# Kernel tuning notes

Measured on AMD Instinct MI355X. Metric: run time of the kernel, lower is better.

Reference implementation:

```python
import jax, jax.numpy as jnp
import numpy as np

N_NODES = 10000
N_EDGES = 320000
N_GRAPHS = 64
L = 3  # num_layers


def _gru(a, h, wih, whh, bih, bhh):
    # torch.nn.GRUCell math: input a, hidden h
    gi = a @ wih.T + bih
    gh = h @ whh.T + bhh
    ir, iz, inn = jnp.split(gi, 3, axis=-1)
    hr, hz, hn = jnp.split(gh, 3, axis=-1)
    r = jax.nn.sigmoid(ir + hr)
    z = jax.nn.sigmoid(iz + hz)
    n = jnp.tanh(inn + r * hn)
    return (1.0 - z) * n + z * h


def _ggc(x, src, dst, w, wih, whh, bih, bhh):
    # PyG GatedGraphConv: pad features up to out_channels, then L rounds of
    # (linear -> scatter-add over edges -> GRUCell update)
    out_ch = w.shape[-1]
    if x.shape[-1] < out_ch:
        x = jnp.concatenate(
            [x, jnp.zeros((x.shape[0], out_ch - x.shape[-1]), x.dtype)], axis=-1)
    for i in range(w.shape[0]):
        m = x @ w[i]                                        # [N, C]
        a = jax.ops.segment_sum(m[src], dst, num_segments=N_NODES)  # scatter-add
        x = _gru(a, x, wih, whh, bih, bhh)
    return x


def setup_inputs() -> dict:
    key = jax.random.key(0)
    ks = jax.random.split(key, 16)
    d1, d2 = 128, 256
    s1, s2 = 1.0 / np.sqrt(d1), 1.0 / np.sqrt(d2)
    x = jax.random.normal(ks[0], (N_NODES, d1), dtype=jnp.float32)
    edge_index = jax.random.randint(ks[1], (2, N_EDGES), 0, N_NODES, dtype=jnp.int64)
    batch = jnp.sort(jax.random.randint(ks[2], (N_NODES,), 0, N_GRAPHS, dtype=jnp.int64))
    return {
        "x": x,
        "edge_index": edge_index,
        "batch": batch,
        "w1": jax.random.normal(ks[3], (L, d1, d1), jnp.float32) * s1,
        "gru1_wih": jax.random.normal(ks[4], (3 * d1, d1), jnp.float32) * s1,
        "gru1_whh": jax.random.normal(ks[5], (3 * d1, d1), jnp.float32) * s1,
        "gru1_bih": jax.random.normal(ks[6], (3 * d1,), jnp.float32) * s1,
        "gru1_bhh": jax.random.normal(ks[7], (3 * d1,), jnp.float32) * s1,
        "w2": jax.random.normal(ks[8], (L, d2, d2), jnp.float32) * s2,
        "gru2_wih": jax.random.normal(ks[9], (3 * d2, d2), jnp.float32) * s2,
        "gru2_whh": jax.random.normal(ks[10], (3 * d2, d2), jnp.float32) * s2,
        "gru2_bih": jax.random.normal(ks[11], (3 * d2,), jnp.float32) * s2,
        "gru2_bhh": jax.random.normal(ks[12], (3 * d2,), jnp.float32) * s2,
        "fc_w": jax.random.normal(ks[13], (6, d2), jnp.float32) * s2,
        "fc_b": jnp.zeros((6,), jnp.float32),
    }


def reference(x, edge_index, batch, w1, gru1_wih, gru1_whh, gru1_bih, gru1_bhh,
              w2, gru2_wih, gru2_whh, gru2_bih, gru2_bhh, fc_w, fc_b):
    src, dst = edge_index[0], edge_index[1]
    y = jax.nn.relu(_ggc(x, src, dst, w1, gru1_wih, gru1_whh, gru1_bih, gru1_bhh))
    y = _ggc(y, src, dst, w2, gru2_wih, gru2_whh, gru2_bih, gru2_bhh)
    y = jax.ops.segment_max(y, batch, num_segments=N_GRAPHS)  # global max pool [G, 256]
    return y @ fc_w.T + fc_b  # [G, 6]
```

## Files before the change

kernel.cpp:

```cpp
#include <hip/hip_runtime.h>

#define NN 10000
#define NNP 10112
#define NE 320000
#define NG 64
#define D1 128
#define D2 256
#define MT 79
#define MT64 158

typedef unsigned short u16;
typedef short v8s __attribute__((ext_vector_type(8)));
typedef float v4f __attribute__((ext_vector_type(4)));

__device__ __forceinline__ u16 f2bf(float x) {
    unsigned u = __float_as_uint(x);
    return (u16)((u + 0x7fffu + ((u >> 16) & 1u)) >> 16);
}
__device__ __forceinline__ float bf2f(u16 b) {
    return __uint_as_float(((unsigned)b) << 16);
}
__device__ __forceinline__ float sigm(float x) { return 1.f / (1.f + __expf(-x)); }
__device__ __forceinline__ float tanh_f(float x) {
    float cx = fminf(fmaxf(x, -15.f), 15.f);
    float e = __expf(2.f * cx);
    return (e - 1.f) / (e + 1.f);
}

#define MF(d, a, b) d = __builtin_amdgcn_mfma_f32_16x16x32_bf16(a, b, d, 0, 0, 0)

#define GLDS16(gp, lp)                                                         \
    __builtin_amdgcn_global_load_lds(                                          \
        (__attribute__((address_space(1))) unsigned int*)(unsigned long long)(gp), \
        (__attribute__((address_space(3))) unsigned int*)(lp), 16, 0, 0)

#define SWIZZLE(bx, by)                          \
    const int bid_ = blockIdx.x;                 \
    const int l_ = bid_ >> 3;                    \
    const int by = (bid_ & 7) * 10 + l_ % 10;    \
    const int bx = l_ / 10;                      \
    if (by >= MT) return;

__global__ __launch_bounds__(256)
void mm_k(const u16* __restrict__ Ah, const u16* __restrict__ Al,
          const u16* __restrict__ Bh, const u16* __restrict__ Bl,
          float* __restrict__ Cm, int K) {
    const int by = blockIdx.x, bx = blockIdx.y;
    __shared__ u16 lds[16384];
    const int tid = threadIdx.x;
    const int wave = tid >> 6, lane = tid & 63;
    const int wm = (wave >> 1) * 32, wn = (wave & 1) * 32;
    const int bm = by * 64, bn = bx * 64;
    const int quad = lane >> 4, r16 = lane & 15;
    const int NK = K >> 5;

    auto STAGE = [&](int b, int k0) {
        size_t ga = (size_t)(bm + lane) * K + k0 + wave * 8;
        size_t gb = (size_t)(bn + lane) * K + k0 + wave * 8;
        int s = b * 8192 + (wave * 64 + lane) * 8;
        GLDS16(Ah + ga, &lds[s]);
        GLDS16(Al + ga, &lds[2048 + s]);
        GLDS16(Bh + gb, &lds[4096 + s]);
        GLDS16(Bl + gb, &lds[6144 + s]);
    };

    v4f acc[2][2] = {};
    STAGE(0, 0);
    __syncthreads();
    int cur = 0;
    for (int ks = 0; ks < NK; ++ks) {
        if (ks + 1 < NK) STAGE(cur ^ 1, (ks + 1) * 32);
        const int bb = cur * 8192;
        v8s af[2], alf[2], bf[2], blf[2];
#pragma unroll
        for (int i = 0; i < 2; ++i) {
            int ra = bb + (quad * 64 + wm + i * 16 + r16) * 8;
            int rb = bb + (quad * 64 + wn + i * 16 + r16) * 8;
            af[i]  = *(const v8s*)&lds[ra];
            alf[i] = *(const v8s*)&lds[2048 + ra];
            bf[i]  = *(const v8s*)&lds[4096 + rb];
            blf[i] = *(const v8s*)&lds[6144 + rb];
        }
#pragma unroll
        for (int i = 0; i < 2; ++i)
#pragma unroll
            for (int j = 0; j < 2; ++j) {
                MF(acc[i][j], af[i], bf[j]);
                MF(acc[i][j], af[i], blf[j]);
                MF(acc[i][j], alf[i], bf[j]);
            }
        __syncthreads();
        cur ^= 1;
    }
#pragma unroll
    for (int i = 0; i < 2; ++i) {
        int gr0 = bm + wm + i * 16 + quad * 4;
#pragma unroll
        for (int j = 0; j < 2; ++j) {
            int gc = bn + wn + j * 16 + r16;
#pragma unroll
            for (int r = 0; r < 4; ++r) {
                int gr = gr0 + r;
                if (gr < NN) Cm[(size_t)gr * K + gc] = acc[i][j][r];
            }
        }
    }
}

template<int MODE, int OS>
__global__ __launch_bounds__(256)
void giqru_k(const u16* __restrict__ Ah, const u16* __restrict__ Al,
             const u16* __restrict__ Xh, const u16* __restrict__ Xl,
             const u16* __restrict__ WcH, const u16* __restrict__ WcL,
             const float* __restrict__ bih, const float* __restrict__ bhh,
             u16* __restrict__ xh_out, u16* __restrict__ xl_out,
             const int* __restrict__ batch, unsigned* __restrict__ pool,
             int C) {
    SWIZZLE(bx, by)
    __shared__ u16 lds[32768];
    const int tid = threadIdx.x;
    const int wave = tid >> 6, lane = tid & 63;
    const int wm = (wave >> 1) * 64, wn = (wave & 1) * 64;
    const int bm = by * 128, bn = bx * 128;
    const int quad = lane >> 4, r16 = lane & 15;
    const int K2 = 2 * C;
    const int NK = K2 >> 5;

    auto STAGE = [&](int b, int k0) {
        const u16* sh = (k0 < C) ? Ah : Xh;
        const u16* sl = (k0 < C) ? Al : Xl;
        const int kk = (k0 < C) ? k0 : k0 - C;
        const int bb = b * 16384;
#pragma unroll
        for (int j = 0; j < 2; ++j) {
            int row = j * 64 + lane;
            size_t ga = (size_t)(bm + row) * C + kk + wave * 8;
            size_t gb = (size_t)(bn + row) * K2 + k0 + wave * 8;
            int s = bb + (wave * 128 + row) * 8;
            GLDS16(sh + ga, &lds[s]);
            GLDS16(sl + ga, &lds[4096 + s]);
            GLDS16(WcH + gb, &lds[8192 + s]);
            GLDS16(WcL + gb, &lds[12288 + s]);
        }
    };

    v4f acc[4][4] = {};
    STAGE(0, 0);
    __syncthreads();
    int cur = 0;
    for (int ks = 0; ks < NK; ++ks) {
        if (ks + 1 < NK) STAGE(cur ^ 1, (ks + 1) * 32);
        const int bb = cur * 16384;
        v8s bhf[4], blf[4];
#pragma unroll
        for (int j = 0; j < 4; ++j) {
            int rb = bb + (quad * 128 + wn + j * 16 + r16) * 8;
            bhf[j] = *(const v8s*)&lds[8192 + rb];
            blf[j] = *(const v8s*)&lds[12288 + rb];
        }
        const bool aphase = (ks * 32) < C;
#pragma unroll
        for (int i = 0; i < 4; ++i) {
            int ra = bb + (quad * 128 + wm + i * 16 + r16) * 8;
            v8s fah = *(const v8s*)&lds[ra];
            v8s fal = *(const v8s*)&lds[4096 + ra];
            MF(acc[i][0], fah, bhf[0]); MF(acc[i][0], fah, blf[0]); MF(acc[i][0], fal, bhf[0]);
            MF(acc[i][1], fah, bhf[1]); MF(acc[i][1], fah, blf[1]); MF(acc[i][1], fal, bhf[1]);
            if (aphase) {
                MF(acc[i][2], fah, bhf[2]); MF(acc[i][2], fah, blf[2]); MF(acc[i][2], fal, bhf[2]);
            } else {
                MF(acc[i][3], fah, bhf[3]); MF(acc[i][3], fah, blf[3]); MF(acc[i][3], fal, bhf[3]);
            }
        }
        __syncthreads();
        cur ^= 1;
    }

    const int c = bx * 32 + (wn ? 16 : 0) + r16;
    const float br = bih[c] + bhh[c];
    const float bz = bih[C + c] + bhh[C + c];
    const float bi_n = bih[2 * C + c];
    const float bh_n = bhh[2 * C + c];
#pragma unroll
    for (int i = 0; i < 4; ++i) {
        int R0 = bm + wm + i * 16 + quad * 4;
#pragma unroll
        for (int r = 0; r < 4; ++r) {
            int R = R0 + r;
            if (R >= NN) continue;
            float rr = sigm(acc[i][0][r] + br);
            float zz = sigm(acc[i][1][r] + bz);
            float nn_ = tanh_f(acc[i][2][r] + bi_n + rr * (acc[i][3][r] + bh_n));
            float h = bf2f(Xh[(size_t)R * C + c]) + bf2f(Xl[(size_t)R * C + c]);
            float o = (1.f - zz) * nn_ + zz * h;
            if (MODE == 2) {
                unsigned b = __float_as_uint(o);
                unsigned u = (b & 0x80000000u) ? ~b : (b | 0x80000000u);
                atomicMax(&pool[batch[R] * 256 + c], u);
            } else {
                if (MODE == 1) o = fmaxf(o, 0.f);
                u16 hh = f2bf(o);
                xh_out[(size_t)R * OS + c] = hh;
                xl_out[(size_t)R * OS + c] = f2bf(o - bf2f(hh));
            }
        }
    }
}

__global__ void count_k(const int* __restrict__ dst, int* __restrict__ cnt) {
    int e = blockIdx.x * blockDim.x + threadIdx.x;
    if (e < NE) atomicAdd(&cnt[dst[e]], 1);
}

__global__ void scan_k(const int* __restrict__ cnt, int* __restrict__ off,
                       int* __restrict__ cur) {
    __shared__ int ps[1024];
    const int tid = threadIdx.x;
    const int CH = (NN + 1023) / 1024;
    const int base = tid * CH;
    int s = 0;
    for (int i = 0; i < CH; ++i) {
        int idx = base + i;
        if (idx < NN) s += cnt[idx];
    }
    ps[tid] = s;
    __syncthreads();
    for (int d = 1; d < 1024; d <<= 1) {
        int v = (tid >= d) ? ps[tid - d] : 0;
        __syncthreads();
        ps[tid] += v;
        __syncthreads();
    }
    int run = (tid > 0) ? ps[tid - 1] : 0;
    for (int i = 0; i < CH; ++i) {
        int idx = base + i;
        if (idx <= NN) { off[idx] = run; if (idx < NN) cur[idx] = run; }
        if (idx < NN) run += cnt[idx];
    }
}

__global__ void fill_k(const int* __restrict__ src, const int* __restrict__ dst,
                       int* __restrict__ cur, int* __restrict__ elist) {
    int e = blockIdx.x * blockDim.x + threadIdx.x;
    if (e >= NE) return;
    int p = atomicAdd(&cur[dst[e]], 1);
    elist[p] = src[e];
}

template<int C>
__global__ void gather_k(const float* __restrict__ m, const int* __restrict__ off,
                         const int* __restrict__ elist,
                         u16* __restrict__ ah, u16* __restrict__ al) {
    constexpr int LPN = C / 4;
    int t = blockIdx.x * blockDim.x + threadIdx.x;
    int node = t / LPN;
    if (node >= NN) return;
    int c = (t % LPN) * 4;
    int s0 = off[node], s1 = off[node + 1];
    v4f a0 = 0.f, a1 = 0.f, a2 = 0.f, a3 = 0.f;
    int i = s0;
    for (; i + 4 <= s1; i += 4) {
        int e0 = elist[i], e1 = elist[i + 1], e2 = elist[i + 2], e3 = elist[i + 3];
        v4f v0 = *(const v4f*)(m + (size_t)e0 * C + c);
        v4f v1 = *(const v4f*)(m + (size_t)e1 * C + c);
        v4f v2 = *(const v4f*)(m + (size_t)e2 * C + c);
        v4f v3 = *(const v4f*)(m + (size_t)e3 * C + c);
        a0 += v0; a1 += v1; a2 += v2; a3 += v3;
    }
    for (; i < s1; ++i) {
        int e = elist[i];
        a0 += *(const v4f*)(m + (size_t)e * C + c);
    }
    v4f acc = (a0 + a1) + (a2 + a3);
    ushort4 h, l;
    h.x = f2bf(acc[0]); l.x = f2bf(acc[0] - bf2f(h.x));
    h.y = f2bf(acc[1]); l.y = f2bf(acc[1] - bf2f(h.y));
    h.z = f2bf(acc[2]); l.z = f2bf(acc[2] - bf2f(h.z));
    h.w = f2bf(acc[3]); l.w = f2bf(acc[3] - bf2f(h.w));
    *(ushort4*)(ah + (size_t)node * C + c) = h;
    *(ushort4*)(al + (size_t)node * C + c) = l;
}

__global__ void prep_k(const float* __restrict__ w1, const float* __restrict__ w2,
                       const float* __restrict__ wih1, const float* __restrict__ whh1,
                       const float* __restrict__ wih2, const float* __restrict__ whh2,
                       const float* __restrict__ xin,
                       u16* __restrict__ B1h, u16* __restrict__ B1l,
                       u16* __restrict__ B2h, u16* __restrict__ B2l,
                       u16* __restrict__ Wc1h, u16* __restrict__ Wc1l,
                       u16* __restrict__ Wc2h, u16* __restrict__ Wc2l,
                       u16* __restrict__ xh, u16* __restrict__ xl) {
    const int n1 = 3 * D1 * D1;
    const int n2 = 3 * D2 * D2;
    const int c1 = 4 * D1 * 2 * D1;
    const int c2 = 4 * D2 * 2 * D2;
    int t = blockIdx.x * blockDim.x + threadIdx.x;
    if (t < n1) {
        int l = t / (D1 * D1), rem = t - l * (D1 * D1);
        int k = rem / D1, n = rem - k * D1;
        float v = w1[t]; u16 h = f2bf(v);
        int o = (l * D1 + n) * D1 + k;
        B1h[o] = h; B1l[o] = f2bf(v - bf2f(h)); return;
    }
    t -= n1;
    if (t < n2) {
        int l = t / (D2 * D2), rem = t - l * (D2 * D2);
        int k = rem / D2, n = rem - k * D2;
        float v = w2[t]; u16 h = f2bf(v);
        int o = (l * D2 + n) * D2 + k;
        B2h[o] = h; B2l[o] = f2bf(v - bf2f(h)); return;
    }
    t -= n2;
    if (t < c1) {
        int jp = t >> 8, k = t & 255;
        int c = ((jp >> 6) << 4) | (jp & 15);
        int g = (jp >> 4) & 3;
        float v;
        if (g == 0)      v = (k < D1) ? wih1[c * D1 + k]            : whh1[c * D1 + k - D1];
        else if (g == 1) v = (k < D1) ? wih1[(D1 + c) * D1 + k]     : whh1[(D1 + c) * D1 + k - D1];
        else if (g == 2) v = (k < D1) ? wih1[(2 * D1 + c) * D1 + k] : 0.f;
        else             v = (k < D1) ? 0.f : whh1[(2 * D1 + c) * D1 + k - D1];
        u16 h = f2bf(v);
        Wc1h[t] = h; Wc1l[t] = f2bf(v - bf2f(h)); return;
    }
    t -= c1;
    if (t < c2) {
        int jp = t >> 9, k = t & 511;
        int c = ((jp >> 6) << 4) | (jp & 15);
        int g = (jp >> 4) & 3;
        float v;
        if (g == 0)      v = (k < D2) ? wih2[c * D2 + k]            : whh2[c * D2 + k - D2];
        else if (g == 1) v = (k < D2) ? wih2[(D2 + c) * D2 + k]     : whh2[(D2 + c) * D2 + k - D2];
        else if (g == 2) v = (k < D2) ? wih2[(2 * D2 + c) * D2 + k] : 0.f;
        else             v = (k < D2) ? 0.f : whh2[(2 * D2 + c) * D2 + k - D2];
        u16 h = f2bf(v);
        Wc2h[t] = h; Wc2l[t] = f2bf(v - bf2f(h)); return;
    }
    t -= c2;
    if (t < NN * D1) {
        float v = xin[t];
        u16 h = f2bf(v);
        xh[t] = h;
        xl[t] = f2bf(v - bf2f(h));
    }
}

__global__ void pad_k(u16* __restrict__ xh, u16* __restrict__ xl) {
    int t = blockIdx.x * blockDim.x + threadIdx.x;
    if (t >= NN * 128) return;
    int n = t >> 7, c = 128 + (t & 127);
    xh[n * 256 + c] = 0;
    xl[n * 256 + c] = 0;
}

__global__ void pool_init_k(unsigned* __restrict__ pool) {
    int t = blockIdx.x * blockDim.x + threadIdx.x;
    if (t < NG * D2) pool[t] = 0x007FFFFFu;
}

__global__ void fc_k(const unsigned* __restrict__ pool, const float* __restrict__ w,
                     const float* __restrict__ b, float* __restrict__ out) {
    int t = blockIdx.x * blockDim.x + threadIdx.x;
    if (t >= NG * 6) return;
    int g = t / 6, o = t - g * 6;
    float s = b[o];
    for (int c = 0; c < D2; ++c) {
        unsigned u = pool[g * D2 + c];
        unsigned bits = (u & 0x80000000u) ? (u ^ 0x80000000u) : ~u;
        s += __uint_as_float(bits) * w[o * D2 + c];
    }
    out[t] = s;
}

extern "C" void kernel_launch(void* const* d_in, const int* in_sizes, int n_in,
                              void* d_out, int out_size, void* d_ws, size_t ws_size,
                              hipStream_t stream) {
    const float* x_in = (const float*)d_in[0];
    const int* ei = (const int*)d_in[1];
    const int* src = ei;
    const int* dst = ei + NE;
    const int* batch = (const int*)d_in[2];
    const float* w1   = (const float*)d_in[3];
    const float* wih1 = (const float*)d_in[4];
    const float* whh1 = (const float*)d_in[5];
    const float* bih1 = (const float*)d_in[6];
    const float* bhh1 = (const float*)d_in[7];
    const float* w2   = (const float*)d_in[8];
    const float* wih2 = (const float*)d_in[9];
    const float* whh2 = (const float*)d_in[10];
    const float* bih2 = (const float*)d_in[11];
    const float* bhh2 = (const float*)d_in[12];
    const float* fcw  = (const float*)d_in[13];
    const float* fcb  = (const float*)d_in[14];
    float* out = (float*)d_out;

    float* ws = (float*)d_ws;
    float* mbuf = ws;
    u16* a_h  = (u16*)(mbuf + (size_t)NNP * 256);
    u16* a_l  = a_h + (size_t)NNP * 256;
    u16* xA0h = a_l + (size_t)NNP * 256;
    u16* xA0l = xA0h + (size_t)NNP * 128;
    u16* xA1h = xA0l + (size_t)NNP * 128;
    u16* xA1l = xA1h + (size_t)NNP * 128;
    u16* xB0h = xA1l + (size_t)NNP * 128;
    u16* xB0l = xB0h + (size_t)NNP * 256;
    u16* xB1h = xB0l + (size_t)NNP * 256;
    u16* xB1l = xB1h + (size_t)NNP * 256;
    u16* B1h  = xB1l + (size_t)NNP * 256;
    u16* B1l  = B1h + 3 * D1 * D1;
    u16* B2h  = B1l + 3 * D1 * D1;
    u16* B2l  = B2h + 3 * D2 * D2;
    u16* Wc1h = B2l + 3 * D2 * D2;
    u16* Wc1l = Wc1h + 4 * D1 * 2 * D1;
    u16* Wc2h = Wc1l + 4 * D1 * 2 * D1;
    u16* Wc2l = Wc2h + 4 * D2 * 2 * D2;
    int* cnt   = (int*)(Wc2l + 4 * D2 * 2 * D2);
    int* off   = cnt + NN;
    int* cur   = off + NN + 1;
    int* elist = cur + NN;
    unsigned* pool = (unsigned*)(elist + NE);

    hipMemsetAsync(cnt, 0, NN * sizeof(int), stream);
    count_k<<<(NE + 255) / 256, 256, 0, stream>>>(dst, cnt);
    scan_k<<<1, 1024, 0, stream>>>(cnt, off, cur);
    fill_k<<<(NE + 255) / 256, 256, 0, stream>>>(src, dst, cur, elist);
    {
        int total = 3 * D1 * D1 + 3 * D2 * D2 + 4 * D1 * 2 * D1 + 4 * D2 * 2 * D2 + NN * D1;
        prep_k<<<(total + 255) / 256, 256, 0, stream>>>(
            w1, w2, wih1, whh1, wih2, whh2, x_in,
            B1h, B1l, B2h, B2l, Wc1h, Wc1l, Wc2h, Wc2l, xA0h, xA0l);
    }
    pad_k<<<(NN * 128 + 255) / 256, 256, 0, stream>>>(xB0h, xB0l);
    pool_init_k<<<(NG * D2 + 255) / 256, 256, 0, stream>>>(pool);

    const int G1 = 80 * 4;
    const int G2 = 80 * 8;
    const int GG1 = (NN * (D1 / 4) + 255) / 256;
    const int GG2 = (NN * (D2 / 4) + 255) / 256;

    mm_k<<<dim3(MT64, D1 / 64), 256, 0, stream>>>(xA0h, xA0l, B1h, B1l, mbuf, D1);
    gather_k<D1><<<GG1, 256, 0, stream>>>(mbuf, off, elist, a_h, a_l);
    giqru_k<0, 128><<<G1, 256, 0, stream>>>(
        a_h, a_l, xA0h, xA0l, Wc1h, Wc1l, bih1, bhh1,
        xA1h, xA1l, nullptr, nullptr, D1);

    mm_k<<<dim3(MT64, D1 / 64), 256, 0, stream>>>(xA1h, xA1l, B1h + D1 * D1, B1l + D1 * D1, mbuf, D1);
    gather_k<D1><<<GG1, 256, 0, stream>>>(mbuf, off, elist, a_h, a_l);
    giqru_k<0, 128><<<G1, 256, 0, stream>>>(
        a_h, a_l, xA1h, xA1l, Wc1h, Wc1l, bih1, bhh1,
        xA0h, xA0l, nullptr, nullptr, D1);

    mm_k<<<dim3(MT64, D1 / 64), 256, 0, stream>>>(xA0h, xA0l, B1h + 2 * D1 * D1, B1l + 2 * D1 * D1, mbuf, D1);
    gather_k<D1><<<GG1, 256, 0, stream>>>(mbuf, off, elist, a_h, a_l);
    giqru_k<1, 256><<<G1, 256, 0, stream>>>(
        a_h, a_l, xA0h, xA0l, Wc1h, Wc1l, bih1, bhh1,
        xB0h, xB0l, nullptr, nullptr, D1);

    mm_k<<<dim3(MT64, D2 / 64), 256, 0, stream>>>(xB0h, xB0l, B2h, B2l, mbuf, D2);
    gather_k<D2><<<GG2, 256, 0, stream>>>(mbuf, off, elist, a_h, a_l);
    giqru_k<0, 256><<<G2, 256, 0, stream>>>(
        a_h, a_l, xB0h, xB0l, Wc2h, Wc2l, bih2, bhh2,
        xB1h, xB1l, nullptr, nullptr, D2);

    mm_k<<<dim3(MT64, D2 / 64), 256, 0, stream>>>(xB1h, xB1l, B2h + D2 * D2, B2l + D2 * D2, mbuf, D2);
    gather_k<D2><<<GG2, 256, 0, stream>>>(mbuf, off, elist, a_h, a_l);
    giqru_k<0, 256><<<G2, 256, 0, stream>>>(
        a_h, a_l, xB1h, xB1l, Wc2h, Wc2l, bih2, bhh2,
        xB0h, xB0l, nullptr, nullptr, D2);

    mm_k<<<dim3(MT64, D2 / 64), 256, 0, stream>>>(xB0h, xB0l, B2h + 2 * D2 * D2, B2l + 2 * D2 * D2, mbuf, D2);
    gather_k<D2><<<GG2, 256, 0, stream>>>(mbuf, off, elist, a_h, a_l);
    giqru_k<2, 256><<<G2, 256, 0, stream>>>(
        a_h, a_l, xB0h, xB0l, Wc2h, Wc2l, bih2, bhh2,
        nullptr, nullptr, batch, pool, D2);

    fc_k<<<1, 512, 0, stream>>>(pool, fcw, fcb, out);
}
```

Baseline: 677.9 us.

## Store activations and weights in 64-row by 8-column blocked layout for contiguous LDS staging

Switches all bf16 hi/lo activation and weight buffers to a blocked layout (64 or 128 rows by 8 columns as contiguous 1KB/2KB chunks), so each global_load_lds reads a fully contiguous 1KB segment instead of strided rows. The GRU GEMM tile shrinks from 128x128 to 64x128 with smaller LDS, doubling the grid, and mm_k adopts the XCD-aware block swizzle. The point is better coalescing and occupancy, at the cost of more complex index math in the producer kernels and more blocks re-reading weights.

```diff
diff --git a/kernel.cpp b/kernel.cpp
--- a/kernel.cpp
+++ b/kernel.cpp
@@ -6,8 +6,7 @@
 #define NG 64
 #define D1 128
 #define D2 256
-#define MT 79
-#define MT64 158
+#define MT 158
 
 typedef unsigned short u16;
 typedef short v8s __attribute__((ext_vector_type(8)));
@@ -34,18 +33,19 @@
         (__attribute__((address_space(1))) unsigned int*)(unsigned long long)(gp), \
         (__attribute__((address_space(3))) unsigned int*)(lp), 16, 0, 0)
 
-#define SWIZZLE(bx, by)                          \
+#define SWZ(bx, by)                              \
     const int bid_ = blockIdx.x;                 \
     const int l_ = bid_ >> 3;                    \
-    const int by = (bid_ & 7) * 10 + l_ % 10;    \
-    const int bx = l_ / 10;                      \
+    const int by = (bid_ & 7) * 20 + l_ % 20;    \
+    const int bx = l_ / 20;                      \
     if (by >= MT) return;
+
 
 __global__ __launch_bounds__(256)
 void mm_k(const u16* __restrict__ Ah, const u16* __restrict__ Al,
           const u16* __restrict__ Bh, const u16* __restrict__ Bl,
           float* __restrict__ Cm, int K) {
-    const int by = blockIdx.x, bx = blockIdx.y;
+    SWZ(bx, by)
     __shared__ u16 lds[16384];
     const int tid = threadIdx.x;
     const int wave = tid >> 6, lane = tid & 63;
@@ -53,15 +53,25 @@
     const int bm = by * 64, bn = bx * 64;
     const int quad = lane >> 4, r16 = lane & 15;
     const int NK = K >> 5;
+    const size_t arow = (size_t)(bm >> 6) * (K >> 3);
+    const size_t brow = (size_t)(bn >> 6) * (K >> 3);
 
     auto STAGE = [&](int b, int k0) {
-        size_t ga = (size_t)(bm + lane) * K + k0 + wave * 8;
-        size_t gb = (size_t)(bn + lane) * K + k0 + wave * 8;
-        int s = b * 8192 + (wave * 64 + lane) * 8;
-        GLDS16(Ah + ga, &lds[s]);
-        GLDS16(Al + ga, &lds[2048 + s]);
-        GLDS16(Bh + gb, &lds[4096 + s]);
-        GLDS16(Bl + gb, &lds[6144 + s]);
+        const u16* pa_h = Ah + (arow + (k0 >> 3)) * 512;
+        const u16* pa_l = Al + (arow + (k0 >> 3)) * 512;
+        const u16* pb_h = Bh + (brow + (k0 >> 3)) * 512;
+        const u16* pb_l = Bl + (brow + (k0 >> 3)) * 512;
+        const int B = b * 8192;
+#pragma unroll
+        for (int t = 0; t < 4; ++t) {
+            int u = (t << 2) | wave;
+            const u16* gp; int ld;
+            if (u < 4)       { gp = pa_h + u * 512;        ld = B + u * 512; }
+            else if (u < 8)  { gp = pa_l + (u - 4) * 512;  ld = B + 2048 + (u - 4) * 512; }
+            else if (u < 12) { gp = pb_h + (u - 8) * 512;  ld = B + 4096 + (u - 8) * 512; }
+            else             { gp = pb_l + (u - 12) * 512; ld = B + 6144 + (u - 12) * 512; }
+            GLDS16(gp + lane * 8, &lds[ld]);
+        }
     };
 
     v4f acc[2][2] = {};
@@ -69,13 +79,13 @@
     __syncthreads();
     int cur = 0;
     for (int ks = 0; ks < NK; ++ks) {
-        if (ks + 1 < NK) STAGE(cur ^ 1, (ks + 1) * 32);
-        const int bb = cur * 8192;
+        if (ks + 1 < NK) STAGE(cur ^ 1, (ks + 1) << 5);
+        const int B = cur * 8192;
         v8s af[2], alf[2], bf[2], blf[2];
 #pragma unroll
         for (int i = 0; i < 2; ++i) {
-            int ra = bb + (quad * 64 + wm + i * 16 + r16) * 8;
-            int rb = bb + (quad * 64 + wn + i * 16 + r16) * 8;
+            int ra = B + quad * 512 + (wm + i * 16 + r16) * 8;
+            int rb = B + quad * 512 + (wn + i * 16 + r16) * 8;
             af[i]  = *(const v8s*)&lds[ra];
             alf[i] = *(const v8s*)&lds[2048 + ra];
             bf[i]  = *(const v8s*)&lds[4096 + rb];
@@ -116,60 +126,70 @@
              u16* __restrict__ xh_out, u16* __restrict__ xl_out,
              const int* __restrict__ batch, unsigned* __restrict__ pool,
              int C) {
-    SWIZZLE(bx, by)
-    __shared__ u16 lds[32768];
+    SWZ(bx, by)
+    __shared__ u16 lds[24576];
     const int tid = threadIdx.x;
     const int wave = tid >> 6, lane = tid & 63;
-    const int wm = (wave >> 1) * 64, wn = (wave & 1) * 64;
-    const int bm = by * 128, bn = bx * 128;
+    const int wm = (wave >> 1) * 32, wn = (wave & 1) * 64;
+    const int bm = by * 64, bn = bx * 128;
     const int quad = lane >> 4, r16 = lane & 15;
     const int K2 = 2 * C;
     const int NK = K2 >> 5;
+    const int CCH = C >> 3;
+    const size_t arow = (size_t)(bm >> 6) * CCH;
+    const size_t wrow = (size_t)(bn >> 7) * (K2 >> 3);
 
     auto STAGE = [&](int b, int k0) {
-        const u16* sh = (k0 < C) ? Ah : Xh;
-        const u16* sl = (k0 < C) ? Al : Xl;
-        const int kk = (k0 < C) ? k0 : k0 - C;
-        const int bb = b * 16384;
-#pragma unroll
-        for (int j = 0; j < 2; ++j) {
-            int row = j * 64 + lane;
-            size_t ga = (size_t)(bm + row) * C + kk + wave * 8;
-            size_t gb = (size_t)(bn + row) * K2 + k0 + wave * 8;
-            int s = bb + (wave * 128 + row) * 8;
-            GLDS16(sh + ga, &lds[s]);
-            GLDS16(sl + ga, &lds[4096 + s]);
-            GLDS16(WcH + gb, &lds[8192 + s]);
-            GLDS16(WcL + gb, &lds[12288 + s]);
+        const u16* sh; const u16* sl; int kk;
+        if (k0 < C) { sh = Ah; sl = Al; kk = k0; } else { sh = Xh; sl = Xl; kk = k0 - C; }
+        const u16* pa_h = sh + (arow + (kk >> 3)) * 512;
+        const u16* pa_l = sl + (arow + (kk >> 3)) * 512;
+        const u16* pw_h = WcH + (wrow + (k0 >> 3)) * 1024;
+        const u16* pw_l = WcL + (wrow + (k0 >> 3)) * 1024;
+        const int B = b * 12288;
+#pragma unroll
+        for (int t = 0; t < 6; ++t) {
+            int u = (t << 2) | wave;
+            const u16* gp; int ld;
+            if (u < 4)       { gp = pa_h + u * 512;        ld = B + u * 512; }
+            else if (u < 8)  { gp = pa_l + (u - 4) * 512;  ld = B + 2048 + (u - 4) * 512; }
+            else if (u < 16) { gp = pw_h + (u - 8) * 512;  ld = B + 4096 + (u - 8) * 512; }
+            else             { gp = pw_l + (u - 16) * 512; ld = B + 8192 + (u - 16) * 512; }
+            GLDS16(gp + lane * 8, &lds[ld]);
         }
     };
 
-    v4f acc[4][4] = {};
+    v4f acc[2][4] = {};
     STAGE(0, 0);
     __syncthreads();
     int cur = 0;
     for (int ks = 0; ks < NK; ++ks) {
-        if (ks + 1 < NK) STAGE(cur ^ 1, (ks + 1) * 32);
-        const int bb = cur * 16384;
-        v8s bhf[4], blf[4];
-#pragma unroll
-        for (int j = 0; j < 4; ++j) {
-            int rb = bb + (quad * 128 + wn + j * 16 + r16) * 8;
-            bhf[j] = *(const v8s*)&lds[8192 + rb];
-            blf[j] = *(const v8s*)&lds[12288 + rb];
-        }
-        const bool aphase = (ks * 32) < C;
-#pragma unroll
-        for (int i = 0; i < 4; ++i) {
-            int ra = bb + (quad * 128 + wm + i * 16 + r16) * 8;
+        const int k0 = ks << 5;
+        if (ks + 1 < NK) STAGE(cur ^ 1, (ks + 1) << 5);
+        const int B = cur * 12288;
+        const bool ap = (k0 < C);
+        const int g2 = ap ? 2 : 3;
+        v8s w0h, w0l, w1h, w1l, w2h, w2l;
+        {
+            int p0 = B + 4096 + quad * 1024 + (wn + r16) * 8;
+            w0h = *(const v8s*)&lds[p0];
+            w0l = *(const v8s*)&lds[4096 + p0];
+            w1h = *(const v8s*)&lds[p0 + 128];
+            w1l = *(const v8s*)&lds[4096 + p0 + 128];
+            w2h = *(const v8s*)&lds[p0 + g2 * 128];
+            w2l = *(const v8s*)&lds[4096 + p0 + g2 * 128];
+        }
+#pragma unroll
+        for (int i = 0; i < 2; ++i) {
+            int ra = B + quad * 512 + (wm + i * 16 + r16) * 8;
             v8s fah = *(const v8s*)&lds[ra];
-            v8s fal = *(const v8s*)&lds[4096 + ra];
-            MF(acc[i][0], fah, bhf[0]); MF(acc[i][0], fah, blf[0]); MF(acc[i][0], fal, bhf[0]);
-            MF(acc[i][1], fah, bhf[1]); MF(acc[i][1], fah, blf[1]); MF(acc[i][1], fal, bhf[1]);
-            if (aphase) {
-                MF(acc[i][2], fah, bhf[2]); MF(acc[i][2], fah, blf[2]); MF(acc[i][2], fal, bhf[2]);
+            v8s fal = *(const v8s*)&lds[2048 + ra];
+            MF(acc[i][0], fah, w0h); MF(acc[i][0], fah, w0l); MF(acc[i][0], fal, w0h);
+            MF(acc[i][1], fah, w1h); MF(acc[i][1], fah, w1l); MF(acc[i][1], fal, w1h);
+            if (ap) {
+                MF(acc[i][2], fah, w2h); MF(acc[i][2], fah, w2l); MF(acc[i][2], fal, w2h);
             } else {
-                MF(acc[i][3], fah, bhf[3]); MF(acc[i][3], fah, blf[3]); MF(acc[i][3], fal, bhf[3]);
+                MF(acc[i][3], fah, w2h); MF(acc[i][3], fah, w2l); MF(acc[i][3], fal, w2h);
             }
         }
         __syncthreads();
@@ -181,8 +201,9 @@
     const float bz = bih[C + c] + bhh[C + c];
     const float bi_n = bih[2 * C + c];
     const float bh_n = bhh[2 * C + c];
-#pragma unroll
-    for (int i = 0; i < 4; ++i) {
+    const int cch = c >> 3, cr = c & 7;
+#pragma unroll
+    for (int i = 0; i < 2; ++i) {
         int R0 = bm + wm + i * 16 + quad * 4;
 #pragma unroll
         for (int r = 0; r < 4; ++r) {
@@ -191,7 +212,8 @@
             float rr = sigm(acc[i][0][r] + br);
             float zz = sigm(acc[i][1][r] + bz);
             float nn_ = tanh_f(acc[i][2][r] + bi_n + rr * (acc[i][3][r] + bh_n));
-            float h = bf2f(Xh[(size_t)R * C + c]) + bf2f(Xl[(size_t)R * C + c]);
+            size_t hx = ((size_t)(R >> 6) * CCH + cch) * 512 + ((R & 63) << 3) + cr;
+            float h = bf2f(Xh[hx]) + bf2f(Xl[hx]);
             float o = (1.f - zz) * nn_ + zz * h;
             if (MODE == 2) {
                 unsigned b = __float_as_uint(o);
@@ -199,9 +221,10 @@
                 atomicMax(&pool[batch[R] * 256 + c], u);
             } else {
                 if (MODE == 1) o = fmaxf(o, 0.f);
+                size_t ox = ((size_t)(R >> 6) * (OS >> 3) + cch) * 512 + ((R & 63) << 3) + cr;
                 u16 hh = f2bf(o);
-                xh_out[(size_t)R * OS + c] = hh;
-                xl_out[(size_t)R * OS + c] = f2bf(o - bf2f(hh));
+                xh_out[ox] = hh;
+                xl_out[ox] = f2bf(o - bf2f(hh));
             }
         }
     }
@@ -277,8 +300,9 @@
     h.y = f2bf(acc[1]); l.y = f2bf(acc[1] - bf2f(h.y));
     h.z = f2bf(acc[2]); l.z = f2bf(acc[2] - bf2f(h.z));
     h.w = f2bf(acc[3]); l.w = f2bf(acc[3] - bf2f(h.w));
-    *(ushort4*)(ah + (size_t)node * C + c) = h;
-    *(ushort4*)(al + (size_t)node * C + c) = l;
+    size_t ox = ((size_t)(node >> 6) * (C >> 3) + (c >> 3)) * 512 + ((node & 63) << 3) + (c & 7);
+    *(ushort4*)(ah + ox) = h;
+    *(ushort4*)(al + ox) = l;
 }
 
 __global__ void prep_k(const float* __restrict__ w1, const float* __restrict__ w2,
@@ -299,7 +323,7 @@
         int l = t / (D1 * D1), rem = t - l * (D1 * D1);
         int k = rem / D1, n = rem - k * D1;
         float v = w1[t]; u16 h = f2bf(v);
-        int o = (l * D1 + n) * D1 + k;
+        size_t o = l * D1 * D1 + ((size_t)(n >> 6) * (D1 >> 3) + (k >> 3)) * 512 + ((n & 63) << 3) + (k & 7);
         B1h[o] = h; B1l[o] = f2bf(v - bf2f(h)); return;
     }
     t -= n1;
@@ -307,7 +331,7 @@
         int l = t / (D2 * D2), rem = t - l * (D2 * D2);
         int k = rem / D2, n = rem - k * D2;
         float v = w2[t]; u16 h = f2bf(v);
-        int o = (l * D2 + n) * D2 + k;
+        size_t o = l * D2 * D2 + ((size_t)(n >> 6) * (D2 >> 3) + (k >> 3)) * 512 + ((n & 63) << 3) + (k & 7);
         B2h[o] = h; B2l[o] = f2bf(v - bf2f(h)); return;
     }
     t -= n2;
@@ -321,7 +345,8 @@
         else if (g == 2) v = (k < D1) ? wih1[(2 * D1 + c) * D1 + k] : 0.f;
         else             v = (k < D1) ? 0.f : whh1[(2 * D1 + c) * D1 + k - D1];
         u16 h = f2bf(v);
-        Wc1h[t] = h; Wc1l[t] = f2bf(v - bf2f(h)); return;
+        size_t o = ((size_t)(jp >> 7) * 32 + (k >> 3)) * 1024 + ((jp & 127) << 3) + (k & 7);
+        Wc1h[o] = h; Wc1l[o] = f2bf(v - bf2f(h)); return;
     }
     t -= c1;
     if (t < c2) {
@@ -334,23 +359,27 @@
         else if (g == 2) v = (k < D2) ? wih2[(2 * D2 + c) * D2 + k] : 0.f;
         else             v = (k < D2) ? 0.f : whh2[(2 * D2 + c) * D2 + k - D2];
         u16 h = f2bf(v);
-        Wc2h[t] = h; Wc2l[t] = f2bf(v - bf2f(h)); return;
+        size_t o = ((size_t)(jp >> 7) * 64 + (k >> 3)) * 1024 + ((jp & 127) << 3) + (k & 7);
+        Wc2h[o] = h; Wc2l[o] = f2bf(v - bf2f(h)); return;
     }
     t -= c2;
     if (t < NN * D1) {
+        int n = t >> 7, cc = t & 127;
         float v = xin[t];
         u16 h = f2bf(v);
-        xh[t] = h;
-        xl[t] = f2bf(v - bf2f(h));
+        size_t o = ((size_t)(n >> 6) * 16 + (cc >> 3)) * 512 + ((n & 63) << 3) + (cc & 7);
+        xh[o] = h;
+        xl[o] = f2bf(v - bf2f(h));
     }
 }
 
 __global__ void pad_k(u16* __restrict__ xh, u16* __restrict__ xl) {
     int t = blockIdx.x * blockDim.x + threadIdx.x;
-    if (t >= NN * 128) return;
+    if (t >= NNP * 128) return;
     int n = t >> 7, c = 128 + (t & 127);
-    xh[n * 256 + c] = 0;
-    xl[n * 256 + c] = 0;
+    size_t o = ((size_t)(n >> 6) * 32 + (c >> 3)) * 512 + ((n & 63) << 3) + (c & 7);
+    xh[o] = 0;
+    xl[o] = 0;
 }
 
 __global__ void pool_init_k(unsigned* __restrict__ pool) {
@@ -430,45 +459,47 @@
             w1, w2, wih1, whh1, wih2, whh2, x_in,
             B1h, B1l, B2h, B2l, Wc1h, Wc1l, Wc2h, Wc2l, xA0h, xA0l);
     }
-    pad_k<<<(NN * 128 + 255) / 256, 256, 0, stream>>>(xB0h, xB0l);
+    pad_k<<<(NNP * 128 + 255) / 256, 256, 0, stream>>>(xB0h, xB0l);
     pool_init_k<<<(NG * D2 + 255) / 256, 256, 0, stream>>>(pool);
 
-    const int G1 = 80 * 4;
-    const int G2 = 80 * 8;
+    const int M1 = 160 * (D1 / 64);
+    const int M2 = 160 * (D2 / 64);
+    const int G1 = 160 * (D1 / 32);
+    const int G2 = 160 * (D2 / 32);
     const int GG1 = (NN * (D1 / 4) + 255) / 256;
     const int GG2 = (NN * (D2 / 4) + 255) / 256;
 
-    mm_k<<<dim3(MT64, D1 / 64), 256, 0, stream>>>(xA0h, xA0l, B1h, B1l, mbuf, D1);
+    mm_k<<<M1, 256, 0, stream>>>(xA0h, xA0l, B1h, B1l, mbuf, D1);
     gather_k<D1><<<GG1, 256, 0, stream>>>(mbuf, off, elist, a_h, a_l);
     giqru_k<0, 128><<<G1, 256, 0, stream>>>(
         a_h, a_l, xA0h, xA0l, Wc1h, Wc1l, bih1, bhh1,
         xA1h, xA1l, nullptr, nullptr, D1);
 
-    mm_k<<<dim3(MT64, D1 / 64), 256, 0, stream>>>(xA1h, xA1l, B1h + D1 * D1, B1l + D1 * D1, mbuf, D1);
+    mm_k<<<M1, 256, 0, stream>>>(xA1h, xA1l, B1h + D1 * D1, B1l + D1 * D1, mbuf, D1);
     gather_k<D1><<<GG1, 256, 0, stream>>>(mbuf, off, elist, a_h, a_l);
     giqru_k<0, 128><<<G1, 256, 0, stream>>>(
         a_h, a_l, xA1h, xA1l, Wc1h, Wc1l, bih1, bhh1,
         xA0h, xA0l, nullptr, nullptr, D1);
 
-    mm_k<<<dim3(MT64, D1 / 64), 256, 0, stream>>>(xA0h, xA0l, B1h + 2 * D1 * D1, B1l + 2 * D1 * D1, mbuf, D1);
+    mm_k<<<M1, 256, 0, stream>>>(xA0h, xA0l, B1h + 2 * D1 * D1, B1l + 2 * D1 * D1, mbuf, D1);
     gather_k<D1><<<GG1, 256, 0, stream>>>(mbuf, off, elist, a_h, a_l);
     giqru_k<1, 256><<<G1, 256, 0, stream>>>(
         a_h, a_l, xA0h, xA0l, Wc1h, Wc1l, bih1, bhh1,
         xB0h, xB0l, nullptr, nullptr, D1);
 
-    mm_k<<<dim3(MT64, D2 / 64), 256, 0, stream>>>(xB0h, xB0l, B2h, B2l, mbuf, D2);
+    mm_k<<<M2, 256, 0, stream>>>(xB0h, xB0l, B2h, B2l, mbuf, D2);
     gather_k<D2><<<GG2, 256, 0, stream>>>(mbuf, off, elist, a_h, a_l);
     giqru_k<0, 256><<<G2, 256, 0, stream>>>(
         a_h, a_l, xB0h, xB0l, Wc2h, Wc2l, bih2, bhh2,
         xB1h, xB1l, nullptr, nullptr, D2);
 
-    mm_k<<<dim3(MT64, D2 / 64), 256, 0, stream>>>(xB1h, xB1l, B2h + D2 * D2, B2l + D2 * D2, mbuf, D2);
+    mm_k<<<M2, 256, 0, stream>>>(xB1h, xB1l, B2h + D2 * D2, B2l + D2 * D2, mbuf, D2);
     gather_k<D2><<<GG2, 256, 0, stream>>>(mbuf, off, elist, a_h, a_l);
     giqru_k<0, 256><<<G2, 256, 0, stream>>>(
         a_h, a_l, xB1h, xB1l, Wc2h, Wc2l, bih2, bhh2,
         xB0h, xB0l, nullptr, nullptr, D2);
 
-    mm_k<<<dim3(MT64, D2 / 64), 256, 0, stream>>>(xB0h, xB0l, B2h + 2 * D2 * D2, B2l + 2 * D2 * D2, mbuf, D2);
+    mm_k<<<M2, 256, 0, stream>>>(xB0h, xB0l, B2h + 2 * D2 * D2, B2l + 2 * D2 * D2, mbuf, D2);
     gather_k<D2><<<GG2, 256, 0, stream>>>(mbuf, off, elist, a_h, a_l);
     giqru_k<2, 256><<<G2, 256, 0, stream>>>(
         a_h, a_l, xB0h, xB0l, Wc2h, Wc2l, bih2, bhh2,
```

New measurement: 584.3 us. -13.8%, faster.
